# Optimization experiments

Hardware: AMD Instinct MI355X
Metric: run time of the kernel (lower is better)

Reference implementation:

```python
import jax, jax.numpy as jnp
import numpy as np

RESO = 64
VSIZE = 0.3
VOXEL = VSIZE / RESO
HALF = VOXEL / 2.0


def _voxel_xyz():
    line = (np.arange(RESO, dtype=np.float32) * VOXEL + HALF)
    x, y, z = np.meshgrid(line, line, line, indexing='ij')
    return jnp.asarray(np.stack([x, y, z]))  # [3,R,R,R]


def _grid_sample_2d(feats, gx, gy):
    # feats: [NV,C,H,W]; gx,gy: [NV,N] normalized coords (torch align_corners-style)
    NV, C, H, W = feats.shape
    ix = (gx + 1.0) * 0.5 * (W - 1)
    iy = (gy + 1.0) * 0.5 * (H - 1)
    ix0 = jnp.floor(ix); iy0 = jnp.floor(iy)
    ix1 = ix0 + 1.0;     iy1 = iy0 + 1.0
    # bilinear weights from unclamped corners
    w_nw = (ix1 - ix) * (iy1 - iy)
    w_ne = (ix - ix0) * (iy1 - iy)
    w_sw = (ix1 - ix) * (iy - iy0)
    w_se = (ix - ix0) * (iy - iy0)
    mask = ((ix >= 0) & (ix <= W - 1) & (iy >= 0) & (iy <= H - 1)).astype(feats.dtype)
    cx0 = jnp.clip(ix0, 0, W - 1).astype(jnp.int32)
    cx1 = jnp.clip(ix1, 0, W - 1).astype(jnp.int32)
    cy0 = jnp.clip(iy0, 0, H - 1).astype(jnp.int32)
    cy1 = jnp.clip(iy1, 0, H - 1).astype(jnp.int32)
    feats_flat = feats.reshape(NV, C, H * W)  # [NV,C,HW]
    gather = jax.vmap(lambda f, i: f[:, i])   # per-view [C,HW],[N] -> [C,N]
    v_nw = gather(feats_flat, cy0 * W + cx0)
    v_ne = gather(feats_flat, cy0 * W + cx1)
    v_sw = gather(feats_flat, cy1 * W + cx0)
    v_se = gather(feats_flat, cy1 * W + cx1)
    out = (v_nw * w_nw[:, None] + v_ne * w_ne[:, None]
           + v_sw * w_sw[:, None] + v_se * w_se[:, None])  # [NV,C,N]
    return out, mask


def setup_inputs() -> dict:
    key = jax.random.key(0)
    k_feat, k1, k2, k3 = jax.random.split(key, 4)
    NV, C, H, W = 8, 32, 128, 128
    feats = jax.random.normal(k_feat, (NV, C, H, W), dtype=jnp.float32)
    # realistic pinhole intrinsics for a 512x512 image
    K = np.array([[400.0, 0.0, 256.0], [0.0, 400.0, 256.0], [0.0, 0.0, 1.0]], np.float32)
    Ks = jnp.asarray(np.tile(K, (NV, 1, 1)))
    # identity-rotation w2c poses, camera ~0.5m from volume along +z
    poses = []
    for i in range(NV):
        t = np.array([0.02 * (i - 3.5), 0.01 * (i % 2), 0.5 + 0.02 * i], np.float32)
        poses.append(np.concatenate([np.eye(3, dtype=np.float32), t[:, None]], axis=1))
    ref_poses = jnp.asarray(np.stack(poses))
    bbox = jnp.asarray(np.array([[-0.15, -0.15, 0.0], [0.15, 0.15, 0.3]], np.float32))
    W1 = jax.random.normal(k1, (32, 32), dtype=jnp.float32) * 0.1
    W2 = jax.random.normal(k2, (32, 16), dtype=jnp.float32) * 0.1
    W3 = jax.random.normal(k3, (16, 8), dtype=jnp.float32) * 0.1
    return {"feats": feats, "ref_poses": ref_poses, "Ks": Ks, "bbox": bbox,
            "img_h": 512, "img_w": 512,
            "W1": W1, "b1": jnp.zeros((32,), jnp.float32),
            "W2": W2, "b2": jnp.zeros((16,), jnp.float32),
            "W3": W3, "b3": jnp.zeros((8,), jnp.float32)}


def reference(feats, ref_poses, Ks, bbox, img_h, img_w, W1, b1, W2, b2, W3, b3):
    NV, C, H, W = feats.shape
    dt = feats.dtype
    # homogeneous pad of poses and intrinsics
    pose_h = jnp.tile(jnp.eye(4, dtype=dt), (NV, 1, 1)).at[:, :3, :4].set(ref_poses)
    K_pad = jnp.tile(jnp.eye(4, dtype=dt), (NV, 1, 1)).at[:, :3, :3].set(Ks)
    w2pixel = K_pad @ pose_h  # [NV,4,4]
    # voxel centers in world frame
    xyz = _voxel_xyz() + bbox[0][:, None, None, None]  # [3,R,R,R]
    pts = xyz.reshape(3, -1)                            # [3,N], N=R^3
    homo = jnp.concatenate([pts, jnp.ones_like(pts[0:1])], axis=0)  # [4,N]
    pix = jnp.einsum('vij,jn->vin', w2pixel, homo)[:, :3]           # [NV,3,N]
    z = pix[:, 2]                                                    # [NV,N]
    mask_valid_depth = (z > 0).astype(dt)
    uv = pix[:, :2] / z[:, None, :]                                  # [NV,2,N]
    normalizer = jnp.array([img_w, img_h], dtype=dt)
    grid = uv.transpose(0, 2, 1) / normalizer - 1.0                  # [NV,N,2]
    feat, mask = _grid_sample_2d(feats, grid[..., 0], grid[..., 1])  # [NV,C,N],[NV,N]
    mask = mask * mask_valid_depth
    # [NV,C,(X Y Z)] -> [NV,X,Y,Z,C]
    feat = feat.transpose(0, 2, 1).reshape(NV, RESO, RESO, RESO, C)
    mask = mask.reshape(NV, RESO, RESO, RESO)
    # NOTE: original normalizes over dim=1 (NumX), replicated faithfully
    weight = mask / (jnp.sum(mask, axis=1, keepdims=True) + 1e-8)
    weight = weight[..., None]  # [NV,R,R,R,1]
    h1 = jax.nn.relu(feat @ W1 + b1)
    h2 = jax.nn.relu(h1 @ W2 + b2)
    comp = h2 @ W3 + b3  # [NV,R,R,R,8]
    mean = jnp.sum(comp * weight, axis=0, keepdims=True)
    var = jnp.sum(weight * (comp - mean) ** 2, axis=0, keepdims=True)
    mv = jnp.concatenate([mean, var], axis=-1)       # [1,R,R,R,16]
    return jnp.transpose(mv, (0, 4, 3, 2, 1))        # [1,16,Z,Y,X]
```

## Files before the change

### kernel.cpp

```cpp
#include <hip/hip_runtime.h>
#include <math.h>

#define NVIEW 8
#define CIN   32
#define HF    128
#define WF    128
#define C1    32
#define C2    16
#define C3    8
#define RESO  64
#define PLANE (HF*WF)

typedef _Float16 half8_t  __attribute__((ext_vector_type(8)));
typedef _Float16 half2_t  __attribute__((ext_vector_type(2)));
typedef float    floatx4  __attribute__((ext_vector_type(4)));

static __device__ __forceinline__ float vox_coord(int idx, float b) {
    const float VOXEL = (float)(0.3 / 64.0);
    const float HALFV = (float)(0.3 / 128.0);
    return (float)idx * VOXEL + HALFV + b;
}

static __device__ __forceinline__ void proj_ixiy(const float* M, float x, float y, float z,
                                                 float& ix, float& iy, float& zc) {
    float u  = fmaf(M[0], x, fmaf(M[1], y, fmaf(M[2],  z, M[3])));
    float vv = fmaf(M[4], x, fmaf(M[5], y, fmaf(M[6],  z, M[7])));
    zc       = fmaf(M[8], x, fmaf(M[9], y, fmaf(M[10], z, M[11])));
    float invz = __builtin_amdgcn_rcpf(zc);
    ix = u * invz;
    iy = vv * invz;
}

static __device__ __forceinline__ void wave_lds_sync() {
    asm volatile("s_waitcnt lgkmcnt(0)" ::: "memory");
}

__global__ void __launch_bounds__(256) k_g(const float* __restrict__ feats,
                                           const float* __restrict__ W1,
                                           const float* __restrict__ b1,
                                           float4* __restrict__ G4,
                                           const float* __restrict__ Ks,
                                           const float* __restrict__ poses,
                                           const int* __restrict__ ihp,
                                           const int* __restrict__ iwp,
                                           const float* __restrict__ W2,
                                           const float* __restrict__ b2,
                                           const float* __restrict__ W3,
                                           const float* __restrict__ b3,
                                           float* __restrict__ mats,
                                           _Float16* __restrict__ w2f,
                                           _Float16* __restrict__ w3f,
                                           float* __restrict__ b2f,
                                           float* __restrict__ b3f) {
    if (blockIdx.x == 512) {
        int t = threadIdx.x;
        if (t < NVIEW * 12) {
            int v = t / 12, rc = t % 12, r = rc / 4, c = rc % 4;
            const float* K = Ks + v * 9;
            const float* P = poses + v * 12;
            float s = K[r*3+0]*P[0*4+c] + K[r*3+1]*P[1*4+c] + K[r*3+2]*P[2*4+c];
            float sc = (r == 0) ? 63.5f / (float)iwp[0]
                     : (r == 1) ? 63.5f / (float)ihp[0] : 1.0f;
            mats[v*12 + r*4 + c] = s * sc;
        }
        if (t < 64) {
            int n = t & 15, g = t >> 4;
#pragma unroll
            for (int jj = 0; jj < 8; jj++) {
                int kk = 8 * g + jj;
                w2f[t*8 + jj] = (_Float16)W2[kk * C2 + n];
                float w3v = (kk < C2 && n < C3) ? W3[kk * C3 + n] : 0.0f;
                w3f[t*8 + jj] = (_Float16)w3v;
            }
            b2f[t] = b2[n];
            b3f[t] = (n < C3) ? b3[n] : 0.0f;
        }
        return;
    }
    int t = blockIdx.x * 256 + threadIdx.x;
    int pix = t & (PLANE - 1);
    int v = t >> 14;
    const float* fp = feats + ((size_t)v * CIN) * PLANE + pix;
    float f[CIN];
#pragma unroll
    for (int c = 0; c < CIN; c++) f[c] = fp[(size_t)c * PLANE];
    float g[C1];
#pragma unroll
    for (int jj = 0; jj < C1; jj++) g[jj] = b1[jj];
#pragma unroll
    for (int c = 0; c < CIN; c++) {
        float fc = f[c];
#pragma unroll
        for (int jj = 0; jj < C1; jj++) g[jj] = fmaf(fc, W1[c*C1 + jj], g[jj]);
    }
#pragma unroll
    for (int q = 0; q < C1/4; q++)
        G4[((size_t)(v * 8 + q)) * PLANE + pix] =
            make_float4(g[4*q], g[4*q+1], g[4*q+2], g[4*q+3]);
}

__global__ void __launch_bounds__(64) k_main(
    const float4* __restrict__ G4,
    const float* __restrict__ mats, const float* __restrict__ bbox,
    const _Float16* __restrict__ w2f, const _Float16* __restrict__ w3f,
    const float* __restrict__ b2f, const float* __restrict__ b3f,
    float* __restrict__ out) {
    __shared__ __align__(16) _Float16 h2h[64 * 24];

    int lane = threadIdx.x;
    int bid  = blockIdx.x;
    int j = bid & 63;
    int k = bid >> 6;
    int m = lane & 15, g = lane >> 4;
    float y = vox_coord(j, bbox[1]);
    float z = vox_coord(k, bbox[2]);

    half8_t w2frag = *(const half8_t*)(w2f + lane * 8);
    half8_t w3frag = *(const half8_t*)(w3f + lane * 8);
    float b2c = b2f[lane];
    float b3c = b3f[lane];
    floatx4 zf4 = {0.0f, 0.0f, 0.0f, 0.0f};

    float M1[16], Msq[16], S16[16];
#pragma unroll
    for (int c = 0; c < 16; c++) { M1[c] = 0.0f; Msq[c] = 0.0f; S16[c] = 0.0f; }

#pragma unroll 1
    for (int v = 0; v < NVIEW; v++) {
        const float* M = mats + v * 12;
        const float4* Gv = G4 + (size_t)v * 8 * PLANE;

        floatx4 c2v[4];
        unsigned int ballo[4];
        int popc = 0;

#pragma unroll
        for (int T = 0; T < 4; T++) {
            int ipt = T * 16 + m;
            float x = vox_coord(ipt, bbox[0]);
            float ix, iy, zc;
            proj_ixiy(M, x, y, z, ix, iy, zc);

            float fx0 = floorf(ix), fy0 = floorf(iy);
            float fx1 = fx0 + 1.0f, fy1 = fy0 + 1.0f;
            bool inb = (ix >= 0.0f) && (ix <= (float)(WF-1)) &&
                       (iy >= 0.0f) && (iy <= (float)(HF-1)) && (zc > 0.0f);
            int cx0 = (int)fminf(fmaxf(fx0, 0.0f), (float)(WF-1));
            int cx1 = (int)fminf(fmaxf(fx1, 0.0f), (float)(WF-1));
            int cy0 = (int)fminf(fmaxf(fy0, 0.0f), (float)(HF-1));
            int cy1 = (int)fminf(fmaxf(fy1, 0.0f), (float)(HF-1));
            float wnw = (fx1 - ix) * (fy1 - iy);
            float wne = (ix - fx0) * (fy1 - iy);
            float wsw = (fx1 - ix) * (iy - fy0);
            float wse = (ix - fx0) * (iy - fy0);

            unsigned long long bal = __ballot(inb);
            ballo[T] = (unsigned int)bal;
            popc += __popcll(bal);

            int t00 = cy0 * WF + cx0, t01 = cy0 * WF + cx1;
            int t10 = cy1 * WF + cx0, t11 = cy1 * WF + cx1;
            const float4* P0 = Gv + (2*g)     * PLANE;
            const float4* P1 = Gv + (2*g + 1) * PLANE;
            float4 a0 = P0[t00], b0 = P0[t01], c0 = P0[t10], d0 = P0[t11];
            float4 a1 = P1[t00], b1v = P1[t01], c1 = P1[t10], d1 = P1[t11];

            float e0 = fmaxf(fmaf(wnw, a0.x, fmaf(wne, b0.x, fmaf(wsw, c0.x, wse * d0.x))), 0.0f);
            float e1 = fmaxf(fmaf(wnw, a0.y, fmaf(wne, b0.y, fmaf(wsw, c0.y, wse * d0.y))), 0.0f);
            float e2 = fmaxf(fmaf(wnw, a0.z, fmaf(wne, b0.z, fmaf(wsw, c0.z, wse * d0.z))), 0.0f);
            float e3 = fmaxf(fmaf(wnw, a0.w, fmaf(wne, b0.w, fmaf(wsw, c0.w, wse * d0.w))), 0.0f);
            float e4 = fmaxf(fmaf(wnw, a1.x, fmaf(wne, b1v.x, fmaf(wsw, c1.x, wse * d1.x))), 0.0f);
            float e5 = fmaxf(fmaf(wnw, a1.y, fmaf(wne, b1v.y, fmaf(wsw, c1.y, wse * d1.y))), 0.0f);
            float e6 = fmaxf(fmaf(wnw, a1.z, fmaf(wne, b1v.z, fmaf(wsw, c1.z, wse * d1.z))), 0.0f);
            float e7 = fmaxf(fmaf(wnw, a1.w, fmaf(wne, b1v.w, fmaf(wsw, c1.w, wse * d1.w))), 0.0f);

            union { half8_t h8; half2_t h2[4]; } u;
            u.h2[0] = __builtin_bit_cast(half2_t, __builtin_amdgcn_cvt_pkrtz(e0, e1));
            u.h2[1] = __builtin_bit_cast(half2_t, __builtin_amdgcn_cvt_pkrtz(e2, e3));
            u.h2[2] = __builtin_bit_cast(half2_t, __builtin_amdgcn_cvt_pkrtz(e4, e5));
            u.h2[3] = __builtin_bit_cast(half2_t, __builtin_amdgcn_cvt_pkrtz(e6, e7));

            c2v[T] = __builtin_amdgcn_mfma_f32_16x16x32_f16(u.h8, w2frag, zf4, 0, 0, 0);
        }

        wave_lds_sync();
#pragma unroll
        for (int T = 0; T < 4; T++) {
#pragma unroll
            for (int r = 0; r < 4; r++) {
                float vv = fmaxf(c2v[T][r] + b2c, 0.0f);
                h2h[(T*16 + g*4 + r) * 24 + m] = (_Float16)vv;
            }
        }
        wave_lds_sync();

        float msr = __builtin_amdgcn_rcpf((float)(popc >> 2) + 1e-8f);
#pragma unroll
        for (int T = 0; T < 4; T++) {
            half8_t a3 = *(const half8_t*)(h2h + (T*16 + m) * 24 + (g & 1) * 8);
            floatx4 c3 = __builtin_amdgcn_mfma_f32_16x16x32_f16(a3, w3frag, zf4, 0, 0, 0);
#pragma unroll
            for (int r = 0; r < 4; r++) {
                float w = ((ballo[T] >> (g*4 + r)) & 1u) ? msr : 0.0f;
                float val = c3[r] + b3c;
                float t1 = w * val;
                S16[T*4+r] += w;
                M1[T*4+r]  += t1;
                Msq[T*4+r]  = fmaf(t1, val, Msq[T*4+r]);
            }
        }
    }

    if (m < C3) {
        size_t base = (size_t)bid * 64;
#pragma unroll
        for (int T = 0; T < 4; T++) {
            float4 mn, vr;
            mn.x = M1[T*4+0]; mn.y = M1[T*4+1]; mn.z = M1[T*4+2]; mn.w = M1[T*4+3];
            vr.x = fmaf(mn.x*mn.x, S16[T*4+0]-2.0f, Msq[T*4+0]);
            vr.y = fmaf(mn.y*mn.y, S16[T*4+1]-2.0f, Msq[T*4+1]);
            vr.z = fmaf(mn.z*mn.z, S16[T*4+2]-2.0f, Msq[T*4+2]);
            vr.w = fmaf(mn.w*mn.w, S16[T*4+3]-2.0f, Msq[T*4+3]);
            size_t ob = base + T*16 + g*4;
            *(float4*)(out + (size_t)m       * 262144 + ob) = mn;
            *(float4*)(out + (size_t)(m + 8) * 262144 + ob) = vr;
        }
    }
}

extern "C" void kernel_launch(void* const* d_in, const int* in_sizes, int n_in,
                              void* d_out, int out_size, void* d_ws, size_t ws_size,
                              hipStream_t stream) {
    const float* feats = (const float*)d_in[0];
    const float* poses = (const float*)d_in[1];
    const float* Ks    = (const float*)d_in[2];
    const float* bbox  = (const float*)d_in[3];
    const int*   img_h = (const int*)d_in[4];
    const int*   img_w = (const int*)d_in[5];
    const float* W1    = (const float*)d_in[6];
    const float* b1    = (const float*)d_in[7];
    const float* W2    = (const float*)d_in[8];
    const float* b2    = (const float*)d_in[9];
    const float* W3    = (const float*)d_in[10];
    const float* b3    = (const float*)d_in[11];
    float* out = (float*)d_out;
    float* ws  = (float*)d_ws;

    float*     mats = ws;
    _Float16*  w2f  = (_Float16*)(ws + 128);
    _Float16*  w3f  = (_Float16*)(ws + 384);
    float*     b2f  = ws + 640;
    float*     b3f  = ws + 704;
    float4*    G4   = (float4*)(ws + 768);

    hipLaunchKernelGGL(k_g, dim3(513), dim3(256), 0, stream,
                       feats, W1, b1, G4, Ks, poses, img_h, img_w,
                       W2, b2, W3, b3, mats, w2f, w3f, b2f, b3f);
    hipLaunchKernelGGL(k_main, dim3(4096), dim3(64), 0, stream,
                       G4, mats, bbox, w2f, w3f, b2f, b3f, out);
}
```

Measured before the change: 141.5 us.

## Project each voxel once per lane and stage layer-1 features through LDS

```diff
diff --git a/kernel.cpp b/kernel.cpp
--- a/kernel.cpp
+++ b/kernel.cpp
@@ -12,7 +12,6 @@
 #define PLANE (HF*WF)
 
 typedef _Float16 half8_t  __attribute__((ext_vector_type(8)));
-typedef _Float16 half2_t  __attribute__((ext_vector_type(2)));
 typedef float    floatx4  __attribute__((ext_vector_type(4)));
 
 static __device__ __forceinline__ float vox_coord(int idx, float b) {
@@ -99,27 +98,34 @@
             make_float4(g[4*q], g[4*q+1], g[4*q+2], g[4*q+3]);
 }
 
-__global__ void __launch_bounds__(64) k_main(
+__global__ void __launch_bounds__(256, 4) k_main(
     const float4* __restrict__ G4,
     const float* __restrict__ mats, const float* __restrict__ bbox,
     const _Float16* __restrict__ w2f, const _Float16* __restrict__ w3f,
     const float* __restrict__ b2f, const float* __restrict__ b3f,
     float* __restrict__ out) {
-    __shared__ __align__(16) _Float16 h2h[64 * 24];
-
-    int lane = threadIdx.x;
-    int bid  = blockIdx.x;
-    int j = bid & 63;
-    int k = bid >> 6;
+    __shared__ __align__(16) char smem[4][5120 + 3072];
+
+    int tid  = threadIdx.x;
+    int wv   = tid >> 6;
+    int lane = tid & 63;
+    int col  = blockIdx.x * 4 + wv;
+    int j  = col & 63;
+    int kz = col >> 6;
+    char*     h1b = smem[wv];
+    _Float16* h2b = (_Float16*)(smem[wv] + 5120);
+
     int m = lane & 15, g = lane >> 4;
+    float x = vox_coord(lane, bbox[0]);
     float y = vox_coord(j, bbox[1]);
-    float z = vox_coord(k, bbox[2]);
+    float z = vox_coord(kz, bbox[2]);
 
     half8_t w2frag = *(const half8_t*)(w2f + lane * 8);
     half8_t w3frag = *(const half8_t*)(w3f + lane * 8);
     float b2c = b2f[lane];
     float b3c = b3f[lane];
-    floatx4 zf4 = {0.0f, 0.0f, 0.0f, 0.0f};
+    floatx4 cb2 = {b2c, b2c, b2c, b2c};
+    floatx4 cb3 = {b3c, b3c, b3c, b3c};
 
     float M1[16], Msq[16], S16[16];
 #pragma unroll
@@ -130,89 +136,82 @@
         const float* M = mats + v * 12;
         const float4* Gv = G4 + (size_t)v * 8 * PLANE;
 
+        float ix, iy, zc;
+        proj_ixiy(M, x, y, z, ix, iy, zc);
+        float fx0 = floorf(ix), fy0 = floorf(iy);
+        float fx1 = fx0 + 1.0f, fy1 = fy0 + 1.0f;
+        bool inb = (ix >= 0.0f) && (ix <= (float)(WF-1)) &&
+                   (iy >= 0.0f) && (iy <= (float)(HF-1)) && (zc > 0.0f);
+        int cx0 = (int)fminf(fmaxf(fx0, 0.0f), (float)(WF-1));
+        int cx1 = (int)fminf(fmaxf(fx1, 0.0f), (float)(WF-1));
+        int cy0 = (int)fminf(fmaxf(fy0, 0.0f), (float)(HF-1));
+        int cy1 = (int)fminf(fmaxf(fy1, 0.0f), (float)(HF-1));
+        float wnw = (fx1 - ix) * (fy1 - iy);
+        float wne = (ix - fx0) * (fy1 - iy);
+        float wsw = (fx1 - ix) * (iy - fy0);
+        float wse = (ix - fx0) * (iy - fy0);
+
+        unsigned long long bal = __ballot(inb);
+        float msr = __builtin_amdgcn_rcpf((float)__popcll(bal) + 1e-8f);
+
+        int t00 = cy0 * WF + cx0, t01 = cy0 * WF + cx1;
+        int t10 = cy1 * WF + cx0, t11 = cy1 * WF + cx1;
+
+        unsigned int st32[16];
+#pragma unroll
+        for (int q = 0; q < 8; q++) {
+            const float4* P = Gv + (size_t)q * PLANE;
+            float4 a = P[t00], b = P[t01], c4 = P[t10], d = P[t11];
+            float e0 = fmaxf(fmaf(wnw, a.x, fmaf(wne, b.x, fmaf(wsw, c4.x, wse * d.x))), 0.0f);
+            float e1 = fmaxf(fmaf(wnw, a.y, fmaf(wne, b.y, fmaf(wsw, c4.y, wse * d.y))), 0.0f);
+            float e2 = fmaxf(fmaf(wnw, a.z, fmaf(wne, b.z, fmaf(wsw, c4.z, wse * d.z))), 0.0f);
+            float e3 = fmaxf(fmaf(wnw, a.w, fmaf(wne, b.w, fmaf(wsw, c4.w, wse * d.w))), 0.0f);
+            st32[2*q+0] = __builtin_bit_cast(unsigned int, __builtin_amdgcn_cvt_pkrtz(e0, e1));
+            st32[2*q+1] = __builtin_bit_cast(unsigned int, __builtin_amdgcn_cvt_pkrtz(e2, e3));
+        }
+        {
+            uint4* dst = (uint4*)(h1b + lane * 80);
+            const uint4* src = (const uint4*)st32;
+            dst[0] = src[0]; dst[1] = src[1]; dst[2] = src[2]; dst[3] = src[3];
+        }
+        wave_lds_sync();
+
         floatx4 c2v[4];
-        unsigned int ballo[4];
-        int popc = 0;
-
-#pragma unroll
-        for (int T = 0; T < 4; T++) {
-            int ipt = T * 16 + m;
-            float x = vox_coord(ipt, bbox[0]);
-            float ix, iy, zc;
-            proj_ixiy(M, x, y, z, ix, iy, zc);
-
-            float fx0 = floorf(ix), fy0 = floorf(iy);
-            float fx1 = fx0 + 1.0f, fy1 = fy0 + 1.0f;
-            bool inb = (ix >= 0.0f) && (ix <= (float)(WF-1)) &&
-                       (iy >= 0.0f) && (iy <= (float)(HF-1)) && (zc > 0.0f);
-            int cx0 = (int)fminf(fmaxf(fx0, 0.0f), (float)(WF-1));
-            int cx1 = (int)fminf(fmaxf(fx1, 0.0f), (float)(WF-1));
-            int cy0 = (int)fminf(fmaxf(fy0, 0.0f), (float)(HF-1));
-            int cy1 = (int)fminf(fmaxf(fy1, 0.0f), (float)(HF-1));
-            float wnw = (fx1 - ix) * (fy1 - iy);
-            float wne = (ix - fx0) * (fy1 - iy);
-            float wsw = (fx1 - ix) * (iy - fy0);
-            float wse = (ix - fx0) * (iy - fy0);
-
-            unsigned long long bal = __ballot(inb);
-            ballo[T] = (unsigned int)bal;
-            popc += __popcll(bal);
-
-            int t00 = cy0 * WF + cx0, t01 = cy0 * WF + cx1;
-            int t10 = cy1 * WF + cx0, t11 = cy1 * WF + cx1;
-            const float4* P0 = Gv + (2*g)     * PLANE;
-            const float4* P1 = Gv + (2*g + 1) * PLANE;
-            float4 a0 = P0[t00], b0 = P0[t01], c0 = P0[t10], d0 = P0[t11];
-            float4 a1 = P1[t00], b1v = P1[t01], c1 = P1[t10], d1 = P1[t11];
-
-            float e0 = fmaxf(fmaf(wnw, a0.x, fmaf(wne, b0.x, fmaf(wsw, c0.x, wse * d0.x))), 0.0f);
-            float e1 = fmaxf(fmaf(wnw, a0.y, fmaf(wne, b0.y, fmaf(wsw, c0.y, wse * d0.y))), 0.0f);
-            float e2 = fmaxf(fmaf(wnw, a0.z, fmaf(wne, b0.z, fmaf(wsw, c0.z, wse * d0.z))), 0.0f);
-            float e3 = fmaxf(fmaf(wnw, a0.w, fmaf(wne, b0.w, fmaf(wsw, c0.w, wse * d0.w))), 0.0f);
-            float e4 = fmaxf(fmaf(wnw, a1.x, fmaf(wne, b1v.x, fmaf(wsw, c1.x, wse * d1.x))), 0.0f);
-            float e5 = fmaxf(fmaf(wnw, a1.y, fmaf(wne, b1v.y, fmaf(wsw, c1.y, wse * d1.y))), 0.0f);
-            float e6 = fmaxf(fmaf(wnw, a1.z, fmaf(wne, b1v.z, fmaf(wsw, c1.z, wse * d1.z))), 0.0f);
-            float e7 = fmaxf(fmaf(wnw, a1.w, fmaf(wne, b1v.w, fmaf(wsw, c1.w, wse * d1.w))), 0.0f);
-
-            union { half8_t h8; half2_t h2[4]; } u;
-            u.h2[0] = __builtin_bit_cast(half2_t, __builtin_amdgcn_cvt_pkrtz(e0, e1));
-            u.h2[1] = __builtin_bit_cast(half2_t, __builtin_amdgcn_cvt_pkrtz(e2, e3));
-            u.h2[2] = __builtin_bit_cast(half2_t, __builtin_amdgcn_cvt_pkrtz(e4, e5));
-            u.h2[3] = __builtin_bit_cast(half2_t, __builtin_amdgcn_cvt_pkrtz(e6, e7));
-
-            c2v[T] = __builtin_amdgcn_mfma_f32_16x16x32_f16(u.h8, w2frag, zf4, 0, 0, 0);
-        }
-
+#pragma unroll
+        for (int T = 0; T < 4; T++) {
+            half8_t aT = *(const half8_t*)(h1b + (T*16 + m) * 80 + g * 16);
+            c2v[T] = __builtin_amdgcn_mfma_f32_16x16x32_f16(aT, w2frag, cb2, 0, 0, 0);
+        }
+#pragma unroll
+        for (int T = 0; T < 4; T++) {
+#pragma unroll
+            for (int r = 0; r < 4; r++) {
+                float vv = fmaxf(c2v[T][r], 0.0f);
+                h2b[(T*16 + g*4 + r) * 24 + m] = (_Float16)vv;
+            }
+        }
         wave_lds_sync();
-#pragma unroll
-        for (int T = 0; T < 4; T++) {
+
+#pragma unroll
+        for (int T = 0; T < 4; T++) {
+            half8_t a3 = *(const half8_t*)(h2b + (T*16 + m) * 24 + (g & 1) * 8);
+            floatx4 c3 = __builtin_amdgcn_mfma_f32_16x16x32_f16(a3, w3frag, cb3, 0, 0, 0);
 #pragma unroll
             for (int r = 0; r < 4; r++) {
-                float vv = fmaxf(c2v[T][r] + b2c, 0.0f);
-                h2h[(T*16 + g*4 + r) * 24 + m] = (_Float16)vv;
-            }
-        }
-        wave_lds_sync();
-
-        float msr = __builtin_amdgcn_rcpf((float)(popc >> 2) + 1e-8f);
-#pragma unroll
-        for (int T = 0; T < 4; T++) {
-            half8_t a3 = *(const half8_t*)(h2h + (T*16 + m) * 24 + (g & 1) * 8);
-            floatx4 c3 = __builtin_amdgcn_mfma_f32_16x16x32_f16(a3, w3frag, zf4, 0, 0, 0);
-#pragma unroll
-            for (int r = 0; r < 4; r++) {
-                float w = ((ballo[T] >> (g*4 + r)) & 1u) ? msr : 0.0f;
-                float val = c3[r] + b3c;
+                int q = T*16 + g*4 + r;
+                float w = ((bal >> q) & 1ull) ? msr : 0.0f;
+                float val = c3[r];
                 float t1 = w * val;
                 S16[T*4+r] += w;
                 M1[T*4+r]  += t1;
                 Msq[T*4+r]  = fmaf(t1, val, Msq[T*4+r]);
             }
         }
+        wave_lds_sync();
     }
 
     if (m < C3) {
-        size_t base = (size_t)bid * 64;
+        size_t base = (size_t)col * 64;
 #pragma unroll
         for (int T = 0; T < 4; T++) {
             float4 mn, vr;
@@ -256,6 +255,6 @@
     hipLaunchKernelGGL(k_g, dim3(513), dim3(256), 0, stream,
                        feats, W1, b1, G4, Ks, poses, img_h, img_w,
                        W2, b2, W3, b3, mats, w2f, w3f, b2f, b3f);
-    hipLaunchKernelGGL(k_main, dim3(4096), dim3(64), 0, stream,
+    hipLaunchKernelGGL(k_main, dim3(1024), dim3(256), 0, stream,
                        G4, mats, bbox, w2f, w3f, b2f, b3f, out);
 }
```

New measurement: 197.5 us. 39.6% more time.
